# Optimization experiments

Measured on AMD Instinct MI355X. Metric: run time of the kernel, lower is better.

The kernel has to match this reference:

```python
import jax, jax.numpy as jnp
import numpy as np

N, E, ND, ED, H, OUT, L, VC = 10000, 160000, 8, 4, 128, 256, 6, 6
HEADS, C = 4, 128  # GATConv: out_channels=128 per head, concat=False -> mean over heads


def _ln(x, g, b, eps=1e-5):
    m = x.mean(-1, keepdims=True)
    v = ((x - m) ** 2).mean(-1, keepdims=True)
    return (x - m) * jax.lax.rsqrt(v + eps) * g + b


def _gat_layer(h, src, dst, e_attr, lw, a_src, a_dst, lew, a_edge, bias):
    # h: [N,H]; e_attr: [Etot,H]; PyG GATConv(heads=4, concat=False, edge_dim=H)
    xh = (h @ lw).reshape(N, HEADS, C)                 # [N,4,128]
    eh = (e_attr @ lew).reshape(-1, HEADS, C)          # [Etot,4,128]
    al_s = jnp.einsum('nhc,hc->nh', xh, a_src)
    al_d = jnp.einsum('nhc,hc->nh', xh, a_dst)
    al_e = jnp.einsum('ehc,hc->eh', eh, a_edge)
    alpha = jax.nn.leaky_relu(al_s[src] + al_d[dst] + al_e, 0.2)  # [Etot,4]
    amax = jax.ops.segment_max(alpha, dst, num_segments=N)
    ex = jnp.exp(alpha - amax[dst])
    den = jax.ops.segment_sum(ex, dst, num_segments=N)
    w = ex / (den[dst] + 1e-16)
    out = jax.ops.segment_sum(xh[src] * w[..., None], dst, num_segments=N)  # [N,4,128]
    return out.mean(axis=1) + bias


def setup_inputs() -> dict:
    key = jax.random.key(0)
    ks = jax.random.split(key, 32)
    s = 0.05
    d = {
        'x': jax.random.normal(ks[0], (N, ND), jnp.float32),
        'edge_index': jax.random.randint(ks[1], (2, E), 0, N),
        'edge_attr': jax.random.uniform(ks[2], (E, ED), jnp.float32),
        'vnf_context': jax.random.normal(ks[3], (1, VC), jnp.float32),
        # node embedding
        'node_w': jax.random.normal(ks[4], (ND, H)) * s, 'node_b': jnp.zeros((H,)),
        # EdgeAttentionLayer
        'ea_proj_w': jax.random.normal(ks[5], (ED, H)) * s, 'ea_proj_b': jnp.zeros((H,)),
        'vnf_w': jax.random.normal(ks[6], (VC, H)) * s, 'vnf_b': jnp.zeros((H,)),
        'att1_w': jax.random.normal(ks[7], (2 * H, H)) * s, 'att1_b': jnp.zeros((H,)),
        'att2_w': jax.random.normal(ks[8], (H, H // 2)) * s, 'att2_b': jnp.zeros((H // 2,)),
        'att3_w': jax.random.normal(ks[9], (H // 2, 1)) * s, 'att3_b': jnp.zeros((1,)),
        # per-layer GATConv params (stacked over L layers)
        'gat_lin_w': jax.random.normal(ks[10], (L, H, HEADS * C)) * s,
        'gat_att_src': jax.random.normal(ks[11], (L, HEADS, C)) * s,
        'gat_att_dst': jax.random.normal(ks[12], (L, HEADS, C)) * s,
        'gat_lin_edge_w': jax.random.normal(ks[13], (L, H, HEADS * C)) * s,
        'gat_att_edge': jax.random.normal(ks[14], (L, HEADS, C)) * s,
        'gat_bias': jnp.zeros((L, C)),
        'ln_scale': jnp.ones((L, H)), 'ln_bias': jnp.zeros((L, H)),
        # output projection
        'out_w': jax.random.normal(ks[15], (H, OUT)) * s, 'out_b': jnp.zeros((OUT,)),
    }
    return d


def reference(x, edge_index, edge_attr, vnf_context, node_w, node_b, ea_proj_w, ea_proj_b,
              vnf_w, vnf_b, att1_w, att1_b, att2_w, att2_b, att3_w, att3_b,
              gat_lin_w, gat_att_src, gat_att_dst, gat_lin_edge_w, gat_att_edge, gat_bias,
              ln_scale, ln_bias, out_w, out_b):
    src, dst = edge_index[0], edge_index[1]
    h = x @ node_w + node_b                                   # [N,128]
    # EdgeAttentionLayer (eval mode, no network_state)
    ef = edge_attr @ ea_proj_w + ea_proj_b                    # [E,128]
    vnf = vnf_context @ vnf_w + vnf_b                         # [1,128]
    comb = jnp.concatenate([ef, jnp.broadcast_to(vnf, (E, H))], axis=-1)
    a = jax.nn.relu(comb @ att1_w + att1_b)
    a = jax.nn.relu(a @ att2_w + att2_b)
    e_gate = jax.nn.sigmoid(a @ att3_w + att3_b)              # [E,1]
    w_edge = ef * e_gate                                      # [E,128]
    # GATConv default add_self_loops=True, fill_value='mean'
    loop = jnp.arange(N)
    src2 = jnp.concatenate([src, loop])
    dst2 = jnp.concatenate([dst, loop])
    e2 = jnp.concatenate([w_edge, jnp.broadcast_to(w_edge.mean(0, keepdims=True), (N, H))], axis=0)
    for l in range(L):
        hc = _gat_layer(h, src2, dst2, e2, gat_lin_w[l], gat_att_src[l], gat_att_dst[l],
                        gat_lin_edge_w[l], gat_att_edge[l], gat_bias[l])
        h = _ln(h + jax.nn.relu(hc), ln_scale[l], ln_bias[l])
    return h @ out_w + out_b                                  # [N,256]
```

## Files before the change

### kernel.cpp

```cpp
#include <hip/hip_runtime.h>
#include <hip/hip_bf16.h>
#include <math.h>

#define Nn 10000
#define Ee 160000
#define ET 170000
#define LL 6

typedef short v8s __attribute__((ext_vector_type(8)));
typedef float v4f __attribute__((ext_vector_type(4)));
typedef float v2f __attribute__((ext_vector_type(2)));

__device__ __forceinline__ unsigned short f2bf(float v) {
    unsigned int b = __float_as_uint(v);
    b += 0x7fffu + ((b >> 16) & 1u);
    return (unsigned short)(b >> 16);
}
__device__ __forceinline__ float bflo(unsigned int u) { return __uint_as_float(u << 16); }
__device__ __forceinline__ float bfhi(unsigned int u) { return __uint_as_float(u & 0xffff0000u); }

__global__ void k_node_embed(const float* __restrict__ x, const float* __restrict__ nw,
                             const float* __restrict__ nb, float* __restrict__ h,
                             unsigned short* __restrict__ hb) {
    int idx = blockIdx.x * 256 + threadIdx.x;
    if (idx >= Nn * 128) return;
    int n = idx >> 7, c = idx & 127;
    const float* xr = x + (size_t)n * 8;
    float acc = nb[c];
#pragma unroll
    for (int k = 0; k < 8; k++) acc += xr[k] * nw[k * 128 + c];
    h[idx] = acc;
    hb[idx] = f2bf(acc);
}

__global__ void k_small(const float* __restrict__ vnfc, const float* __restrict__ vw,
                        const float* __restrict__ vb, const float* __restrict__ eab,
                        const float* __restrict__ a1w, const float* __restrict__ a1b,
                        const float* __restrict__ eaw, float* __restrict__ E1) {
    __shared__ float vr[128];
    __shared__ float sM1[512];
    __shared__ float sd1[128];
    int t = threadIdx.x;
    if (t < 128) {
        float a = vb[t];
#pragma unroll
        for (int k = 0; k < 6; k++) a += vnfc[k] * vw[k * 128 + t];
        vr[t] = a;
    }
    __syncthreads();
    if (t < 128) {
        float a = a1b[t];
        for (int k = 0; k < 128; k++) a += eab[k] * a1w[k * 128 + t];
        for (int k = 0; k < 128; k++) a += vr[k] * a1w[(128 + k) * 128 + t];
        sd1[t] = a;
    }
    {
        int r = t >> 7, j = t & 127;
        float a = 0.f;
        for (int k = 0; k < 128; k++) a += eaw[r * 128 + k] * a1w[k * 128 + j];
        sM1[r * 128 + j] = a;
    }
    __syncthreads();
    if (t < 128) {
        E1[t * 8 + 0] = sM1[t];
        E1[t * 8 + 1] = sM1[128 + t];
        E1[t * 8 + 2] = sM1[256 + t];
        E1[t * 8 + 3] = sM1[384 + t];
        E1[t * 8 + 4] = sd1[t];
        E1[t * 8 + 5] = 0.f; E1[t * 8 + 6] = 0.f; E1[t * 8 + 7] = 0.f;
    }
}

__global__ void k_bmat(const float* __restrict__ glw, const float* __restrict__ gas,
                       const float* __restrict__ gad, const float* __restrict__ glew,
                       const float* __restrict__ gae, float* __restrict__ Bs,
                       float* __restrict__ Bd, float* __restrict__ Be) {
    int idx = blockIdx.x * 256 + threadIdx.x;
    if (idx >= LL * 128 * 4) return;
    int hh = idx & 3, k = (idx >> 2) & 127, l = idx >> 9;
    const float* lwp = glw  + (size_t)l * 65536 + k * 512 + hh * 128;
    const float* lep = glew + (size_t)l * 65536 + k * 512 + hh * 128;
    const float* sp = gas + l * 512 + hh * 128;
    const float* dp = gad + l * 512 + hh * 128;
    const float* ep = gae + l * 512 + hh * 128;
    float s1 = 0, s2 = 0, s3 = 0;
    for (int c = 0; c < 128; c++) {
        float lv = lwp[c];
        s1 += lv * sp[c];
        s2 += lv * dp[c];
        s3 += lep[c] * ep[c];
    }
    Bs[idx] = s1; Bd[idx] = s2; Be[idx] = s3;
}

__global__ void k_wsum(const float* __restrict__ glw, unsigned short* __restrict__ WsumT) {
    int idx = blockIdx.x * 256 + threadIdx.x;
    if (idx >= LL * 128 * 512) return;
    int kk = idx & 511;
    int c = (idx >> 9) & 127;
    int l = idx >> 16;
    float v = 0.25f * glw[(size_t)l * 65536 + (size_t)(kk & 127) * 512 + (kk >> 7) * 128 + c];
    WsumT[(size_t)l * 65536 + (size_t)c * 512 + kk] = f2bf(v);
}

__global__ void k_w2b(const float* __restrict__ a2w, unsigned short* __restrict__ w2bf) {
    int idx = blockIdx.x * 256 + threadIdx.x;
    if (idx >= 8192) return;
    int j = idx & 7, lane = (idx >> 3) & 63, nt = (idx >> 9) & 3, ks = idx >> 11;
    int k = ks * 32 + ((lane >> 4) << 3) + j;
    int n = nt * 16 + (lane & 15);
    w2bf[idx] = f2bf(a2w[k * 64 + n]);
}

__global__ void k_pb(const float* __restrict__ eaw, const float* __restrict__ eab,
                     const float* __restrict__ Be, float* __restrict__ PB,
                     float* __restrict__ cB) {
    int t = threadIdx.x;
    if (t >= 24) return;
    int l = t >> 2, hh = t & 3;
    const float* bp = Be + l * 512 + hh;
    float s0 = 0, s1 = 0, s2 = 0, s3 = 0, sc = 0;
    for (int k = 0; k < 128; k++) {
        float bv = bp[k * 4];
        s0 += eaw[0 * 128 + k] * bv;
        s1 += eaw[1 * 128 + k] * bv;
        s2 += eaw[2 * 128 + k] * bv;
        s3 += eaw[3 * 128 + k] * bv;
        sc += eab[k] * bv;
    }
    PB[0 * 24 + t] = s0; PB[1 * 24 + t] = s1;
    PB[2 * 24 + t] = s2; PB[3 * 24 + t] = s3;
    cB[t] = sc;
}

__global__ __launch_bounds__(256, 2) void k_edge(
    const float* __restrict__ ea, const float* __restrict__ E1,
    const unsigned short* __restrict__ w2bf,
    const float* __restrict__ a2b, const float* __restrict__ a3w,
    const float* __restrict__ a3b,
    const float* __restrict__ PB, const float* __restrict__ cB,
    float* __restrict__ aleT, float* __restrict__ gsum) {
    __shared__ float4 sM[128];
    __shared__ float sD[128];
    __shared__ float4 sevs[256];
    __shared__ float gsh[256];
    __shared__ float sgsum[5];
    int t = threadIdx.x;
    int lane = t & 63;
    int wid = t >> 6;
    int c = lane & 15, q = lane >> 4;
    int eb0 = blockIdx.x * 256;

    sevs[t] = *(const float4*)(ea + (size_t)(eb0 + t) * 4);
    if (t < 128) {
        int slot = t ^ ((t >> 3) & 3);
        sM[slot] = *(const float4*)(E1 + t * 8);
        sD[t] = E1[t * 8 + 4];
    }
    if (t < 5) sgsum[t] = 0.f;
    __syncthreads();

    float4 ev4[4];
#pragma unroll
    for (int mt = 0; mt < 4; mt++) ev4[mt] = sevs[(wid * 4 + mt) * 16 + c];

    v8s av[4][4];
#pragma unroll
    for (int ks = 0; ks < 4; ks++) {
        float4 mr[8]; float dr[8];
#pragma unroll
        for (int j = 0; j < 8; j++) {
            int k = ks * 32 + q * 8 + j;
            mr[j] = sM[k ^ q];
            dr[j] = sD[k];
        }
#pragma unroll
        for (int mt = 0; mt < 4; mt++) {
            float4 ev = ev4[mt];
            v8s a;
#pragma unroll
            for (int j = 0; j < 8; j++) {
                float xv = fmaxf(dr[j] + ev.x * mr[j].x + ev.y * mr[j].y
                                       + ev.z * mr[j].z + ev.w * mr[j].w, 0.f);
                a[j] = (short)f2bf(xv);
            }
            av[mt][ks] = a;
        }
    }

    v4f acc[4][4];
#pragma unroll
    for (int nt = 0; nt < 4; nt++) {
        float bb = a2b[nt * 16 + c];
#pragma unroll
        for (int mt = 0; mt < 4; mt++) acc[mt][nt] = (v4f){bb, bb, bb, bb};
    }
#pragma unroll
    for (int nt = 0; nt < 4; nt++) {
#pragma unroll
        for (int ks = 0; ks < 4; ks++) {
            v8s b = *(const v8s*)(w2bf + ((size_t)(ks * 4 + nt) * 64 + lane) * 8);
#pragma unroll
            for (int mt = 0; mt < 4; mt++)
                acc[mt][nt] = __builtin_amdgcn_mfma_f32_16x16x32_bf16(av[mt][ks], b, acc[mt][nt], 0, 0, 0);
        }
    }

    float a3r[4];
#pragma unroll
    for (int nt = 0; nt < 4; nt++) a3r[nt] = a3w[nt * 16 + c];
    float a3b0 = a3b[0];
#pragma unroll
    for (int mt = 0; mt < 4; mt++) {
#pragma unroll
        for (int r = 0; r < 4; r++) {
            float s = 0.f;
#pragma unroll
            for (int nt = 0; nt < 4; nt++) s += fmaxf(acc[mt][nt][r], 0.f) * a3r[nt];
            s += __shfl_xor(s, 1); s += __shfl_xor(s, 2);
            s += __shfl_xor(s, 4); s += __shfl_xor(s, 8);
            if (c == 0) gsh[(wid * 4 + mt) * 16 + q * 4 + r] = 1.f / (1.f + __expf(-(s + a3b0)));
        }
    }
    __syncthreads();

    float g = gsh[t];
    float4 evv = sevs[t];
    float v0 = g, v1 = g * evv.x, v2 = g * evv.y, v3 = g * evv.z, v4 = g * evv.w;
#pragma unroll
    for (int d = 32; d > 0; d >>= 1) {
        v0 += __shfl_down(v0, d); v1 += __shfl_down(v1, d); v2 += __shfl_down(v2, d);
        v3 += __shfl_down(v3, d); v4 += __shfl_down(v4, d);
    }
    if (lane == 0) {
        atomicAdd(&sgsum[0], v0); atomicAdd(&sgsum[1], v1); atomicAdd(&sgsum[2], v2);
        atomicAdd(&sgsum[3], v3); atomicAdd(&sgsum[4], v4);
    }
    __syncthreads();
    if (t < 5) atomicAdd(&gsum[t], sgsum[t]);
#pragma unroll
    for (int i4 = 0; i4 < 6; i4++) {
        float4 cc = *(const float4*)(cB + i4 * 4);
        float4 p0 = *(const float4*)(PB + 0 * 24 + i4 * 4);
        float4 p1 = *(const float4*)(PB + 1 * 24 + i4 * 4);
        float4 p2 = *(const float4*)(PB + 2 * 24 + i4 * 4);
        float4 p3 = *(const float4*)(PB + 3 * 24 + i4 * 4);
        float4 o;
        o.x = g * (cc.x + evv.x * p0.x + evv.y * p1.x + evv.z * p2.x + evv.w * p3.x);
        o.y = g * (cc.y + evv.x * p0.y + evv.y * p1.y + evv.z * p2.y + evv.w * p3.y);
        o.z = g * (cc.z + evv.x * p0.z + evv.y * p1.z + evv.z * p2.z + evv.w * p3.z);
        o.w = g * (cc.w + evv.x * p0.w + evv.y * p1.w + evv.z * p2.w + evv.w * p3.w);
        *(float4*)(aleT + (size_t)i4 * Ee * 4 + (size_t)(eb0 + t) * 4) = o;
    }
}

__global__ void k_lale(const float* __restrict__ gsum, const float* __restrict__ PB,
                       const float* __restrict__ cB, float* __restrict__ lale) {
    int t = threadIdx.x;
    if (t >= 24) return;
    float s = gsum[0] * cB[t] + gsum[1] * PB[t] + gsum[2] * PB[24 + t]
            + gsum[3] * PB[48 + t] + gsum[4] * PB[72 + t];
    lale[t] = s * (1.0f / Ee);
}

__global__ void k_hist(const int* __restrict__ ei, int* __restrict__ hist) {
    int i = blockIdx.x * 256 + threadIdx.x;
    if (i >= ET) return;
    int d = (i < Ee) ? ei[Ee + i] : (i - Ee);
    atomicAdd(&hist[d], 1);
}

__global__ __launch_bounds__(1024) void k_scan(const int* __restrict__ hist,
                                               int* __restrict__ seg, int* __restrict__ pos) {
    __shared__ int wsums[16];
    __shared__ int carry_s;
    int t = threadIdx.x;
    int lane = t & 63, wid = t >> 6;
    if (t == 0) { carry_s = 0; seg[0] = 0; }
    __syncthreads();
    for (int base = 0; base < Nn; base += 1024) {
        int idx = base + t;
        int v = (idx < Nn) ? hist[idx] : 0;
        int sc = v;
#pragma unroll
        for (int d = 1; d < 64; d <<= 1) {
            int up = __shfl_up(sc, d);
            if (lane >= d) sc += up;
        }
        if (lane == 63) wsums[wid] = sc;
        __syncthreads();
        if (wid == 0) {
            int wv = (lane < 16) ? wsums[lane] : 0;
            int wsc = wv;
#pragma unroll
            for (int d = 1; d < 16; d <<= 1) {
                int up = __shfl_up(wsc, d);
                if (lane >= d) wsc += up;
            }
            if (lane < 16) wsums[lane] = wsc - wv;
        }
        __syncthreads();
        int carry = carry_s;
        int inc = sc + wsums[wid] + carry;
        if (idx < Nn) { seg[idx + 1] = inc; pos[idx] = inc - v; }
        __syncthreads();
        if (t == 1023) carry_s = inc;
        __syncthreads();
    }
}

__global__ void k_scatter(const int* __restrict__ ei, int* __restrict__ pos,
                          int2* __restrict__ pse) {
    int i = blockIdx.x * 256 + threadIdx.x;
    if (i >= ET) return;
    int s, d;
    if (i < Ee) { s = ei[i]; d = ei[Ee + i]; } else { s = d = i - Ee; }
    int idx = atomicAdd(&pos[d], 1);
    pse[idx] = make_int2(s, i);
}

__global__ void k_ab(const float* __restrict__ h, const float* __restrict__ Bs_l,
                     const float* __restrict__ Bd_l, float* __restrict__ als,
                     float* __restrict__ ald) {
    int idx = blockIdx.x * 256 + threadIdx.x;
    if (idx >= Nn * 8) return;
    int n = idx >> 3, slot = idx & 7;
    const float* B = (slot < 4) ? Bs_l : Bd_l;
    int hh = slot & 3;
    const float4* hr = (const float4*)(h + (size_t)n * 128);
    float s = 0.f;
#pragma unroll 8
    for (int kb = 0; kb < 32; kb++) {
        float4 hv = hr[kb];
        s += hv.x * B[(4 * kb + 0) * 4 + hh] + hv.y * B[(4 * kb + 1) * 4 + hh]
           + hv.z * B[(4 * kb + 2) * 4 + hh] + hv.w * B[(4 * kb + 3) * 4 + hh];
    }
    if (slot < 4) als[n * 4 + hh] = s;
    else          ald[n * 4 + hh] = s;
}

__global__ __launch_bounds__(256) void k_agg3(
    const int2* __restrict__ pse, const int* __restrict__ seg,
    const float* __restrict__ als, const float* __restrict__ ald,
    const float* __restrict__ aleT_l, const float* __restrict__ lale_l,
    const unsigned short* __restrict__ hb, unsigned short* __restrict__ aggb) {
    __shared__ float part[2][512];
    __shared__ float pden[2][4];
    int t = threadIdx.x;
    int lane = t & 63;
    int wv = (t >> 6) & 1;
    int w = t >> 7;
    int n = blockIdx.x * 2 + w;
    int start = seg[n], end = seg[n + 1];
    int deg = end - start;
    int half = (deg + 1) >> 1;
    int s0 = start + wv * half;
    int e0 = wv ? end : start + half;
    int hp = lane >> 4;
    int cch = (lane & 15) * 8;
    float aldh = ald[n * 4 + hp];
    float llh = lale_l[hp];
    float den = 0.f;
    float4 acc0 = make_float4(0.f, 0.f, 0.f, 0.f);
    float4 acc1 = make_float4(0.f, 0.f, 0.f, 0.f);
    int i = s0;
    for (; i + 2 <= e0; i += 2) {
        int2 sa = pse[i], sb = pse[i + 1];
        float ala = sa.y < Ee ? aleT_l[(size_t)sa.y * 4 + hp] : llh;
        float alb = sb.y < Ee ? aleT_l[(size_t)sb.y * 4 + hp] : llh;
        float ava = als[sa.x * 4 + hp] + aldh + ala;
        float avb = als[sb.x * 4 + hp] + aldh + alb;
        ava = ava > 0.f ? ava : 0.2f * ava;
        avb = avb > 0.f ? avb : 0.2f * avb;
        float ea = __expf(fminf(ava, 60.f));
        float eb = __expf(fminf(avb, 60.f));
        den += ea + eb;
        uint4 ua = *(const uint4*)(hb + (size_t)sa.x * 128 + cch);
        uint4 ub = *(const uint4*)(hb + (size_t)sb.x * 128 + cch);
        acc0.x += ea * bflo(ua.x) + eb * bflo(ub.x);
        acc0.y += ea * bfhi(ua.x) + eb * bfhi(ub.x);
        acc0.z += ea * bflo(ua.y) + eb * bflo(ub.y);
        acc0.w += ea * bfhi(ua.y) + eb * bfhi(ub.y);
        acc1.x += ea * bflo(ua.z) + eb * bflo(ub.z);
        acc1.y += ea * bfhi(ua.z) + eb * bfhi(ub.z);
        acc1.z += ea * bflo(ua.w) + eb * bflo(ub.w);
        acc1.w += ea * bfhi(ua.w) + eb * bfhi(ub.w);
    }
    if (i < e0) {
        int2 sa = pse[i];
        float ala = sa.y < Ee ? aleT_l[(size_t)sa.y * 4 + hp] : llh;
        float ava = als[sa.x * 4 + hp] + aldh + ala;
        ava = ava > 0.f ? ava : 0.2f * ava;
        float ea = __expf(fminf(ava, 60.f));
        den += ea;
        uint4 ua = *(const uint4*)(hb + (size_t)sa.x * 128 + cch);
        acc0.x += ea * bflo(ua.x); acc0.y += ea * bfhi(ua.x);
        acc0.z += ea * bflo(ua.y); acc0.w += ea * bfhi(ua.y);
        acc1.x += ea * bflo(ua.z); acc1.y += ea * bfhi(ua.z);
        acc1.z += ea * bflo(ua.w); acc1.w += ea * bfhi(ua.w);
    }
    if (wv == 1) {
        *(float4*)&part[w][lane * 8] = acc0;
        *(float4*)&part[w][lane * 8 + 4] = acc1;
        if ((lane & 15) == 0) pden[w][hp] = den;
    }
    __syncthreads();
    if (wv == 0) {
        float4 p0 = *(const float4*)&part[w][lane * 8];
        float4 p1 = *(const float4*)&part[w][lane * 8 + 4];
        float inv = 1.f / (den + pden[w][hp] + 1e-16f);
        acc0.x = (acc0.x + p0.x) * inv; acc0.y = (acc0.y + p0.y) * inv;
        acc0.z = (acc0.z + p0.z) * inv; acc0.w = (acc0.w + p0.w) * inv;
        acc1.x = (acc1.x + p1.x) * inv; acc1.y = (acc1.y + p1.y) * inv;
        acc1.z = (acc1.z + p1.z) * inv; acc1.w = (acc1.w + p1.w) * inv;
        ushort4 q0, q1;
        q0.x = f2bf(acc0.x); q0.y = f2bf(acc0.y); q0.z = f2bf(acc0.z); q0.w = f2bf(acc0.w);
        q1.x = f2bf(acc1.x); q1.y = f2bf(acc1.y); q1.z = f2bf(acc1.z); q1.w = f2bf(acc1.w);
        *(ushort4*)(aggb + (size_t)n * 512 + lane * 8) = q0;
        *(ushort4*)(aggb + (size_t)n * 512 + lane * 8 + 4) = q1;
    }
}

__global__ __launch_bounds__(256) void k_post(
    const unsigned short* __restrict__ aggb, const unsigned short* __restrict__ WsumT_l,
    const float* __restrict__ gbias, const float* __restrict__ lnsc,
    const float* __restrict__ lnbi, float* __restrict__ h,
    unsigned short* __restrict__ hb, const float* __restrict__ Bs_n,
    const float* __restrict__ Bd_n, float* __restrict__ als, float* __restrict__ ald) {
    int t = threadIdx.x;
    int lane = t & 63, w = t >> 6;
    int n0 = (blockIdx.x * 4 + w) * 16;
    if (n0 >= Nn) return;
    int m = lane & 15, q = lane >> 4;
    v4f acc[8];
#pragma unroll
    for (int nt = 0; nt < 8; nt++) acc[nt] = (v4f){0.f, 0.f, 0.f, 0.f};
    const unsigned short* arow = aggb + (size_t)(n0 + m) * 512 + q * 8;
#pragma unroll 4
    for (int ks = 0; ks < 16; ks++) {
        v8s fa = *(const v8s*)(arow + ks * 32);
#pragma unroll
        for (int nt = 0; nt < 8; nt++) {
            int col = nt * 16 + m;
            v8s fb = *(const v8s*)(WsumT_l + (size_t)col * 512 + ks * 32 + q * 8);
            acc[nt] = __builtin_amdgcn_mfma_f32_16x16x32_bf16(fa, fb, acc[nt], 0, 0, 0);
        }
    }
    float v[8][4];
    float s1[4] = {0.f, 0.f, 0.f, 0.f}, s2[4] = {0.f, 0.f, 0.f, 0.f};
#pragma unroll
    for (int nt = 0; nt < 8; nt++) {
        int col = nt * 16 + m;
        float b = gbias[col];
#pragma unroll
        for (int r = 0; r < 4; r++) {
            int row = n0 + q * 4 + r;
            float val = h[(size_t)row * 128 + col] + fmaxf(acc[nt][r] + b, 0.f);
            v[nt][r] = val;
            s1[r] += val; s2[r] += val * val;
        }
    }
#pragma unroll
    for (int d = 1; d <= 8; d <<= 1) {
#pragma unroll
        for (int r = 0; r < 4; r++) {
            s1[r] += __shfl_xor(s1[r], d);
            s2[r] += __shfl_xor(s2[r], d);
        }
    }
    float o8[8][4];
#pragma unroll
    for (int r = 0; r < 4; r++) {
        float mean = s1[r] * (1.f / 128.f);
        float var = s2[r] * (1.f / 128.f) - mean * mean;
        float rinv = rsqrtf(var + 1e-5f);
        int row = n0 + q * 4 + r;
#pragma unroll
        for (int nt = 0; nt < 8; nt++) {
            int col = nt * 16 + m;
            float o = (v[nt][r] - mean) * rinv * lnsc[col] + lnbi[col];
            o8[nt][r] = o;
            h[(size_t)row * 128 + col] = o;
            hb[(size_t)row * 128 + col] = f2bf(o);
        }
    }
    float sal[4][4], sad[4][4];
#pragma unroll
    for (int r = 0; r < 4; r++) {
#pragma unroll
        for (int hh = 0; hh < 4; hh++) { sal[r][hh] = 0.f; sad[r][hh] = 0.f; }
    }
#pragma unroll
    for (int nt = 0; nt < 8; nt++) {
        int col = nt * 16 + m;
        float4 bs = *(const float4*)(Bs_n + col * 4);
        float4 bd = *(const float4*)(Bd_n + col * 4);
#pragma unroll
        for (int r = 0; r < 4; r++) {
            float o = o8[nt][r];
            sal[r][0] += o * bs.x; sal[r][1] += o * bs.y;
            sal[r][2] += o * bs.z; sal[r][3] += o * bs.w;
            sad[r][0] += o * bd.x; sad[r][1] += o * bd.y;
            sad[r][2] += o * bd.z; sad[r][3] += o * bd.w;
        }
    }
#pragma unroll
    for (int d = 1; d <= 8; d <<= 1) {
#pragma unroll
        for (int r = 0; r < 4; r++) {
#pragma unroll
            for (int hh = 0; hh < 4; hh++) {
                sal[r][hh] += __shfl_xor(sal[r][hh], d);
                sad[r][hh] += __shfl_xor(sad[r][hh], d);
            }
        }
    }
    if (m < 8) {
        int hh = m & 3;
#pragma unroll
        for (int r = 0; r < 4; r++) {
            int row = n0 + q * 4 + r;
            float va = (hh == 0) ? sal[r][0] : (hh == 1) ? sal[r][1] : (hh == 2) ? sal[r][2] : sal[r][3];
            float vd = (hh == 0) ? sad[r][0] : (hh == 1) ? sad[r][1] : (hh == 2) ? sad[r][2] : sad[r][3];
            if (m < 4) als[row * 4 + hh] = va;
            else       ald[row * 4 + hh] = vd;
        }
    }
}

__global__ __launch_bounds__(256) void k_out(
    const float* __restrict__ h, const float* __restrict__ ow,
    const float* __restrict__ ob, float* __restrict__ out) {
    __shared__ float4 hs4[8][32];
    int t = threadIdx.x;
    int n0 = blockIdx.x * 8;
    if (t < 256) {
        int i = t >> 5, kb = t & 31;
        hs4[i][kb] = *(const float4*)(h + (size_t)(n0 + i) * 128 + 4 * kb);
    }
    __syncthreads();
    float acc[8] = {0, 0, 0, 0, 0, 0, 0, 0};
    for (int kb = 0; kb < 32; kb++) {
        float w0 = ow[(4 * kb + 0) * 256 + t];
        float w1 = ow[(4 * kb + 1) * 256 + t];
        float w2 = ow[(4 * kb + 2) * 256 + t];
        float w3 = ow[(4 * kb + 3) * 256 + t];
#pragma unroll
        for (int i = 0; i < 8; i++) {
            float4 hv = hs4[i][kb];
            acc[i] += hv.x * w0 + hv.y * w1 + hv.z * w2 + hv.w * w3;
        }
    }
    float b = ob[t];
#pragma unroll
    for (int i = 0; i < 8; i++) out[(size_t)(n0 + i) * 256 + t] = acc[i] + b;
}

extern "C" void kernel_launch(void* const* d_in, const int* in_sizes, int n_in,
                              void* d_out, int out_size, void* d_ws, size_t ws_size,
                              hipStream_t stream) {
    const float* x    = (const float*)d_in[0];
    const int*   ei   = (const int*)d_in[1];
    const float* ea   = (const float*)d_in[2];
    const float* vnfc = (const float*)d_in[3];
    const float* nw   = (const float*)d_in[4];
    const float* nb   = (const float*)d_in[5];
    const float* eaw  = (const float*)d_in[6];
    const float* eab  = (const float*)d_in[7];
    const float* vw   = (const float*)d_in[8];
    const float* vb   = (const float*)d_in[9];
    const float* a1w  = (const float*)d_in[10];
    const float* a1b  = (const float*)d_in[11];
    const float* a2w  = (const float*)d_in[12];
    const float* a2b  = (const float*)d_in[13];
    const float* a3w  = (const float*)d_in[14];
    const float* a3b  = (const float*)d_in[15];
    const float* glw  = (const float*)d_in[16];
    const float* gas  = (const float*)d_in[17];
    const float* gad  = (const float*)d_in[18];
    const float* glew = (const float*)d_in[19];
    const float* gae  = (const float*)d_in[20];
    const float* gb   = (const float*)d_in[21];
    const float* lnsc = (const float*)d_in[22];
    const float* lnbi = (const float*)d_in[23];
    const float* ow   = (const float*)d_in[24];
    const float* ob   = (const float*)d_in[25];
    float* out = (float*)d_out;

    char* w = (char*)d_ws;
    size_t o = 0;
    auto allocf = [&](size_t cnt) { float* p = (float*)(w + o); o += ((cnt * 4 + 255) / 256) * 256; return p; };
    auto alloci = [&](size_t cnt) { int* p = (int*)(w + o); o += ((cnt * 4 + 255) / 256) * 256; return p; };
    auto allocu = [&](size_t cnt) { unsigned short* p = (unsigned short*)(w + o); o += ((cnt * 2 + 255) / 256) * 256; return p; };
    float* h      = allocf((size_t)Nn * 128);
    unsigned short* hb    = allocu((size_t)Nn * 128);
    unsigned short* aggb  = allocu((size_t)Nn * 512);
    unsigned short* WsumT = allocu((size_t)LL * 128 * 512);
    unsigned short* w2bf  = allocu(8192);
    float* als    = allocf((size_t)Nn * 4);
    float* ald    = allocf((size_t)Nn * 4);
    float* aleT   = allocf((size_t)LL * Ee * 4);
    float* Bs     = allocf(3072);
    float* Bd     = allocf(3072);
    float* Be     = allocf(3072);
    float* E1     = allocf(1024);
    float* PB     = allocf(96);
    float* cB     = allocf(24);
    float* gsum   = allocf(8);
    float* lale   = allocf(32);
    int* seg  = alloci(Nn + 1);
    int* hist = alloci(Nn);
    int* pos  = alloci(Nn);
    int2* pse = (int2*)alloci((size_t)ET * 2);

    hipMemsetAsync(hist, 0, Nn * sizeof(int), stream);
    hipMemsetAsync(gsum, 0, 8 * sizeof(float), stream);

    k_node_embed<<<(Nn * 128 + 255) / 256, 256, 0, stream>>>(x, nw, nb, h, hb);
    k_small<<<1, 512, 0, stream>>>(vnfc, vw, vb, eab, a1w, a1b, eaw, E1);
    k_bmat<<<(LL * 128 * 4 + 255) / 256, 256, 0, stream>>>(glw, gas, gad, glew, gae, Bs, Bd, Be);
    k_wsum<<<(LL * 128 * 512 + 255) / 256, 256, 0, stream>>>(glw, WsumT);
    k_w2b<<<32, 256, 0, stream>>>(a2w, w2bf);
    k_pb<<<1, 32, 0, stream>>>(eaw, eab, Be, PB, cB);
    k_edge<<<Ee / 256, 256, 0, stream>>>(ea, E1, w2bf, a2b, a3w, a3b, PB, cB, aleT, gsum);
    k_hist<<<(ET + 255) / 256, 256, 0, stream>>>(ei, hist);
    k_scan<<<1, 1024, 0, stream>>>(hist, seg, pos);
    k_scatter<<<(ET + 255) / 256, 256, 0, stream>>>(ei, pos, pse);
    k_lale<<<1, 32, 0, stream>>>(gsum, PB, cB, lale);
    k_ab<<<(Nn * 8 + 255) / 256, 256, 0, stream>>>(h, Bs, Bd, als, ald);
    for (int l = 0; l < LL; l++) {
        int ln = (l + 1) % LL;
        k_agg3<<<Nn / 2, 256, 0, stream>>>(pse, seg, als, ald, aleT + (size_t)l * Ee * 4,
                                           lale + l * 4, hb, aggb);
        k_post<<<(625 + 3) / 4, 256, 0, stream>>>(aggb, WsumT + (size_t)l * 65536,
                                                  gb + l * 128, lnsc + l * 128, lnbi + l * 128,
                                                  h, hb, Bs + ln * 512, Bd + ln * 512, als, ald);
    }
    k_out<<<Nn / 8, 256, 0, stream>>>(h, ow, ob, out);
}
```

Before: 515.2 us.

## Split edge attention exp into separate kernel and simplify aggregation to one wave per node

Moves the per-edge leaky-relu and exp computation out of the aggregation kernel into a new edge-parallel kernel that writes exp values for all four heads. Each edge's attention is then computed once instead of being recomputed by all 16 lanes of a head group. The aggregation kernel now uses one wave per node with a 4-way unrolled gather, which removes the two-wave split and the LDS reduction. The cost is an extra kernel launch per layer plus an extra global write and read of the exp values, and high-degree nodes now run on a single wave.

```diff
diff --git a/kernel.cpp b/kernel.cpp
--- a/kernel.cpp
+++ b/kernel.cpp
@@ -310,13 +310,16 @@
 }
 
 __global__ void k_scatter(const int* __restrict__ ei, int* __restrict__ pos,
-                          int2* __restrict__ pse) {
+                          int2* __restrict__ pse, int* __restrict__ srcv,
+                          int* __restrict__ dstv) {
     int i = blockIdx.x * 256 + threadIdx.x;
     if (i >= ET) return;
     int s, d;
     if (i < Ee) { s = ei[i]; d = ei[Ee + i]; } else { s = d = i - Ee; }
     int idx = atomicAdd(&pos[d], 1);
     pse[idx] = make_int2(s, i);
+    srcv[idx] = s;
+    dstv[idx] = d;
 }
 
 __global__ void k_ab(const float* __restrict__ h, const float* __restrict__ Bs_l,
@@ -339,86 +342,80 @@
     else          ald[n * 4 + hh] = s;
 }
 
-__global__ __launch_bounds__(256) void k_agg3(
-    const int2* __restrict__ pse, const int* __restrict__ seg,
+__global__ __launch_bounds__(256) void k_alpha(
+    const int2* __restrict__ pse, const int* __restrict__ dstv,
     const float* __restrict__ als, const float* __restrict__ ald,
     const float* __restrict__ aleT_l, const float* __restrict__ lale_l,
-    const unsigned short* __restrict__ hb, unsigned short* __restrict__ aggb) {
-    __shared__ float part[2][512];
-    __shared__ float pden[2][4];
-    int t = threadIdx.x;
-    int lane = t & 63;
-    int wv = (t >> 6) & 1;
-    int w = t >> 7;
-    int n = blockIdx.x * 2 + w;
+    float* __restrict__ exv) {
+    int i = blockIdx.x * 256 + threadIdx.x;
+    if (i >= ET) return;
+    int2 se = pse[i];
+    int d = dstv[i];
+    float4 as = *(const float4*)(als + (size_t)se.x * 4);
+    float4 ad = *(const float4*)(ald + (size_t)d * 4);
+    float4 ae = (se.y < Ee) ? *(const float4*)(aleT_l + (size_t)se.y * 4)
+                            : *(const float4*)lale_l;
+    float4 o;
+    float a;
+    a = as.x + ad.x + ae.x; a = a > 0.f ? a : 0.2f * a; o.x = __expf(fminf(a, 60.f));
+    a = as.y + ad.y + ae.y; a = a > 0.f ? a : 0.2f * a; o.y = __expf(fminf(a, 60.f));
+    a = as.z + ad.z + ae.z; a = a > 0.f ? a : 0.2f * a; o.z = __expf(fminf(a, 60.f));
+    a = as.w + ad.w + ae.w; a = a > 0.f ? a : 0.2f * a; o.w = __expf(fminf(a, 60.f));
+    *(float4*)(exv + (size_t)i * 4) = o;
+}
+
+__global__ __launch_bounds__(256, 6) void k_agg3(
+    const int* __restrict__ srcv, const int* __restrict__ seg,
+    const float* __restrict__ exv, const unsigned short* __restrict__ hb,
+    unsigned short* __restrict__ aggb) {
+    int t = threadIdx.x;
+    int lane = t & 63, w = t >> 6;
+    int n = blockIdx.x * 4 + w;
     int start = seg[n], end = seg[n + 1];
-    int deg = end - start;
-    int half = (deg + 1) >> 1;
-    int s0 = start + wv * half;
-    int e0 = wv ? end : start + half;
     int hp = lane >> 4;
     int cch = (lane & 15) * 8;
-    float aldh = ald[n * 4 + hp];
-    float llh = lale_l[hp];
     float den = 0.f;
     float4 acc0 = make_float4(0.f, 0.f, 0.f, 0.f);
     float4 acc1 = make_float4(0.f, 0.f, 0.f, 0.f);
-    int i = s0;
-    for (; i + 2 <= e0; i += 2) {
-        int2 sa = pse[i], sb = pse[i + 1];
-        float ala = sa.y < Ee ? aleT_l[(size_t)sa.y * 4 + hp] : llh;
-        float alb = sb.y < Ee ? aleT_l[(size_t)sb.y * 4 + hp] : llh;
-        float ava = als[sa.x * 4 + hp] + aldh + ala;
-        float avb = als[sb.x * 4 + hp] + aldh + alb;
-        ava = ava > 0.f ? ava : 0.2f * ava;
-        avb = avb > 0.f ? avb : 0.2f * avb;
-        float ea = __expf(fminf(ava, 60.f));
-        float eb = __expf(fminf(avb, 60.f));
-        den += ea + eb;
-        uint4 ua = *(const uint4*)(hb + (size_t)sa.x * 128 + cch);
-        uint4 ub = *(const uint4*)(hb + (size_t)sb.x * 128 + cch);
-        acc0.x += ea * bflo(ua.x) + eb * bflo(ub.x);
-        acc0.y += ea * bfhi(ua.x) + eb * bfhi(ub.x);
-        acc0.z += ea * bflo(ua.y) + eb * bflo(ub.y);
-        acc0.w += ea * bfhi(ua.y) + eb * bfhi(ub.y);
-        acc1.x += ea * bflo(ua.z) + eb * bflo(ub.z);
-        acc1.y += ea * bfhi(ua.z) + eb * bfhi(ub.z);
-        acc1.z += ea * bflo(ua.w) + eb * bflo(ub.w);
-        acc1.w += ea * bfhi(ua.w) + eb * bfhi(ub.w);
-    }
-    if (i < e0) {
-        int2 sa = pse[i];
-        float ala = sa.y < Ee ? aleT_l[(size_t)sa.y * 4 + hp] : llh;
-        float ava = als[sa.x * 4 + hp] + aldh + ala;
-        ava = ava > 0.f ? ava : 0.2f * ava;
-        float ea = __expf(fminf(ava, 60.f));
-        den += ea;
-        uint4 ua = *(const uint4*)(hb + (size_t)sa.x * 128 + cch);
-        acc0.x += ea * bflo(ua.x); acc0.y += ea * bfhi(ua.x);
-        acc0.z += ea * bflo(ua.y); acc0.w += ea * bfhi(ua.y);
-        acc1.x += ea * bflo(ua.z); acc1.y += ea * bfhi(ua.z);
-        acc1.z += ea * bflo(ua.w); acc1.w += ea * bfhi(ua.w);
-    }
-    if (wv == 1) {
-        *(float4*)&part[w][lane * 8] = acc0;
-        *(float4*)&part[w][lane * 8 + 4] = acc1;
-        if ((lane & 15) == 0) pden[w][hp] = den;
-    }
-    __syncthreads();
-    if (wv == 0) {
-        float4 p0 = *(const float4*)&part[w][lane * 8];
-        float4 p1 = *(const float4*)&part[w][lane * 8 + 4];
-        float inv = 1.f / (den + pden[w][hp] + 1e-16f);
-        acc0.x = (acc0.x + p0.x) * inv; acc0.y = (acc0.y + p0.y) * inv;
-        acc0.z = (acc0.z + p0.z) * inv; acc0.w = (acc0.w + p0.w) * inv;
-        acc1.x = (acc1.x + p1.x) * inv; acc1.y = (acc1.y + p1.y) * inv;
-        acc1.z = (acc1.z + p1.z) * inv; acc1.w = (acc1.w + p1.w) * inv;
-        ushort4 q0, q1;
-        q0.x = f2bf(acc0.x); q0.y = f2bf(acc0.y); q0.z = f2bf(acc0.z); q0.w = f2bf(acc0.w);
-        q1.x = f2bf(acc1.x); q1.y = f2bf(acc1.y); q1.z = f2bf(acc1.z); q1.w = f2bf(acc1.w);
-        *(ushort4*)(aggb + (size_t)n * 512 + lane * 8) = q0;
-        *(ushort4*)(aggb + (size_t)n * 512 + lane * 8 + 4) = q1;
-    }
+    int i = start;
+    for (; i + 4 <= end; i += 4) {
+        int s0 = srcv[i], s1 = srcv[i + 1], s2 = srcv[i + 2], s3 = srcv[i + 3];
+        float e0 = exv[(size_t)(i + 0) * 4 + hp];
+        float e1 = exv[(size_t)(i + 1) * 4 + hp];
+        float e2 = exv[(size_t)(i + 2) * 4 + hp];
+        float e3 = exv[(size_t)(i + 3) * 4 + hp];
+        uint4 u0 = *(const uint4*)(hb + (size_t)s0 * 128 + cch);
+        uint4 u1 = *(const uint4*)(hb + (size_t)s1 * 128 + cch);
+        uint4 u2 = *(const uint4*)(hb + (size_t)s2 * 128 + cch);
+        uint4 u3 = *(const uint4*)(hb + (size_t)s3 * 128 + cch);
+        den += (e0 + e1) + (e2 + e3);
+        acc0.x += (e0 * bflo(u0.x) + e1 * bflo(u1.x)) + (e2 * bflo(u2.x) + e3 * bflo(u3.x));
+        acc0.y += (e0 * bfhi(u0.x) + e1 * bfhi(u1.x)) + (e2 * bfhi(u2.x) + e3 * bfhi(u3.x));
+        acc0.z += (e0 * bflo(u0.y) + e1 * bflo(u1.y)) + (e2 * bflo(u2.y) + e3 * bflo(u3.y));
+        acc0.w += (e0 * bfhi(u0.y) + e1 * bfhi(u1.y)) + (e2 * bfhi(u2.y) + e3 * bfhi(u3.y));
+        acc1.x += (e0 * bflo(u0.z) + e1 * bflo(u1.z)) + (e2 * bflo(u2.z) + e3 * bflo(u3.z));
+        acc1.y += (e0 * bfhi(u0.z) + e1 * bfhi(u1.z)) + (e2 * bfhi(u2.z) + e3 * bfhi(u3.z));
+        acc1.z += (e0 * bflo(u0.w) + e1 * bflo(u1.w)) + (e2 * bflo(u2.w) + e3 * bflo(u3.w));
+        acc1.w += (e0 * bfhi(u0.w) + e1 * bfhi(u1.w)) + (e2 * bfhi(u2.w) + e3 * bfhi(u3.w));
+    }
+    for (; i < end; i++) {
+        int s0 = srcv[i];
+        float e0 = exv[(size_t)i * 4 + hp];
+        uint4 u0 = *(const uint4*)(hb + (size_t)s0 * 128 + cch);
+        den += e0;
+        acc0.x += e0 * bflo(u0.x); acc0.y += e0 * bfhi(u0.x);
+        acc0.z += e0 * bflo(u0.y); acc0.w += e0 * bfhi(u0.y);
+        acc1.x += e0 * bflo(u0.z); acc1.y += e0 * bfhi(u0.z);
+        acc1.z += e0 * bflo(u0.w); acc1.w += e0 * bfhi(u0.w);
+    }
+    float inv = 1.f / (den + 1e-16f);
+    ushort4 q0, q1;
+    q0.x = f2bf(acc0.x * inv); q0.y = f2bf(acc0.y * inv);
+    q0.z = f2bf(acc0.z * inv); q0.w = f2bf(acc0.w * inv);
+    q1.x = f2bf(acc1.x * inv); q1.y = f2bf(acc1.y * inv);
+    q1.z = f2bf(acc1.z * inv); q1.w = f2bf(acc1.w * inv);
+    *(ushort4*)(aggb + (size_t)n * 512 + lane * 8) = q0;
+    *(ushort4*)(aggb + (size_t)n * 512 + lane * 8 + 4) = q1;
 }
 
 __global__ __launch_bounds__(256) void k_post(
@@ -600,6 +597,7 @@
     float* als    = allocf((size_t)Nn * 4);
     float* ald    = allocf((size_t)Nn * 4);
     float* aleT   = allocf((size_t)LL * Ee * 4);
+    float* exv    = allocf((size_t)ET * 4);
     float* Bs     = allocf(3072);
     float* Bd     = allocf(3072);
     float* Be     = allocf(3072);
@@ -611,6 +609,8 @@
     int* seg  = alloci(Nn + 1);
     int* hist = alloci(Nn);
     int* pos  = alloci(Nn);
+    int* srcv = alloci(ET);
+    int* dstv = alloci(ET);
     int2* pse = (int2*)alloci((size_t)ET * 2);
 
     hipMemsetAsync(hist, 0, Nn * sizeof(int), stream);
@@ -625,13 +625,14 @@
     k_edge<<<Ee / 256, 256, 0, stream>>>(ea, E1, w2bf, a2b, a3w, a3b, PB, cB, aleT, gsum);
     k_hist<<<(ET + 255) / 256, 256, 0, stream>>>(ei, hist);
     k_scan<<<1, 1024, 0, stream>>>(hist, seg, pos);
-    k_scatter<<<(ET + 255) / 256, 256, 0, stream>>>(ei, pos, pse);
+    k_scatter<<<(ET + 255) / 256, 256, 0, stream>>>(ei, pos, pse, srcv, dstv);
     k_lale<<<1, 32, 0, stream>>>(gsum, PB, cB, lale);
     k_ab<<<(Nn * 8 + 255) / 256, 256, 0, stream>>>(h, Bs, Bd, als, ald);
     for (int l = 0; l < LL; l++) {
         int ln = (l + 1) % LL;
-        k_agg3<<<Nn / 2, 256, 0, stream>>>(pse, seg, als, ald, aleT + (size_t)l * Ee * 4,
-                                           lale + l * 4, hb, aggb);
+        k_alpha<<<(ET + 255) / 256, 256, 0, stream>>>(pse, dstv, als, ald,
+                                                      aleT + (size_t)l * Ee * 4, lale + l * 4, exv);
+        k_agg3<<<Nn / 4, 256, 0, stream>>>(srcv, seg, exv, hb, aggb);
         k_post<<<(625 + 3) / 4, 256, 0, stream>>>(aggb, WsumT + (size_t)l * 65536,
                                                   gb + l * 128, lnsc + l * 128, lnbi + l * 128,
                                                   h, hb, Bs + ln * 512, Bd + ln * 512, als, ald);
```

After: 537.7 us. 4.4% more time.
